# Kernel tuning notes

Hardware: AMD Instinct MI355X
Metric: run time of the kernel (lower is better)

The kernel has to match this reference:

```python
import jax, jax.numpy as jnp
import numpy as np

B, IN, H = 16384, 512, 512


def setup_inputs() -> dict:
    key = jax.random.key(0)
    ks = jax.random.split(key, 7)
    s_in = 1.0 / np.sqrt(IN)
    s_h = 1.0 / np.sqrt(H)
    return {
        "x": jax.random.normal(ks[0], (B, IN), jnp.float32),
        "h": jax.random.normal(ks[1], (B, H), jnp.float32),
        "c": jax.random.normal(ks[2], (B, H), jnp.float32),
        # packed gate weights, order [i, f, g, o] along last dim (4*H)
        "Wx": jax.random.normal(ks[3], (IN, 4 * H), jnp.float32) * s_in,
        "Wh": jax.random.normal(ks[4], (H, 4 * H), jnp.float32) * s_h,
        "bx": jax.random.normal(ks[5], (4 * H,), jnp.float32) * s_in,
        "bh": jax.random.normal(ks[6], (4 * H,), jnp.float32) * s_h,
    }


def reference(x, h, c, Wx, Wh, bx, bh):
    # one fused GEMM per input stream instead of 8 small linears; same math
    gates = x @ Wx + bx + h @ Wh + bh          # [B, 4H]
    gi, gf, gg, go = jnp.split(gates, 4, axis=-1)
    i = jax.nn.sigmoid(gi)
    f = jax.nn.sigmoid(gf)
    g = jnp.tanh(gg)
    o = jax.nn.sigmoid(go)
    c_new = f * c + i * g
    h_new = o * jnp.tanh(c_new)
    return (h_new, c_new)
```

## Files before the change

kernel.cpp:

```cpp
#include <hip/hip_runtime.h>
#include <hip/hip_bf16.h>

#define B_DIM   16384
#define IN_DIM  512
#define H_DIM   512
#define K_DIM   1024
#define N4H     2048
#define BH      (B_DIM * H_DIM)

typedef __attribute__((ext_vector_type(8))) short  short8;
typedef __attribute__((ext_vector_type(4))) short  short4v;
typedef __attribute__((ext_vector_type(4))) float  f32x4;

__device__ inline void async_load16(const void* g, void* l) {
    __builtin_amdgcn_global_load_lds(
        (const __attribute__((address_space(1))) void*)g,
        (__attribute__((address_space(3)))       void*)l, 16, 0, 0);
}

__device__ inline short bf16bits(float f) {
    __hip_bfloat16 b = __float2bfloat16(f);
    return *reinterpret_cast<short*>(&b);
}

__device__ inline float sigmoidf_(float v) {
    return 1.0f / (1.0f + __expf(-v));
}
__device__ inline float tanhf_(float v) {
    v = fminf(fmaxf(v, -30.f), 30.f);
    float e = __expf(2.f * v);
    return (e - 1.f) / (e + 1.f);
}

__global__ __launch_bounds__(256) void prep_all(
    const float* __restrict__ Wx, const float* __restrict__ Wh,
    const float* __restrict__ bx, const float* __restrict__ bh,
    const float* __restrict__ x,  const float* __restrict__ h,
    __hip_bfloat16* __restrict__ Wt, __hip_bfloat16* __restrict__ Axh,
    float* __restrict__ bias_p) {
    const int bid = blockIdx.x;
    const int t   = threadIdx.x;

    if (bid < 2048) {
        __shared__ __hip_bfloat16 tile[32][33];
        const int bk = bid & 31;
        const int bn = bid >> 5;
        const int kb = bk * 32, nb = bn * 32;
#pragma unroll
        for (int r = 0; r < 4; ++r) {
            int k_loc = r * 8 + (t >> 5);
            int n_loc = t & 31;
            int kg = kb + k_loc;
            float v = (kg < IN_DIM) ? Wx[(size_t)kg * N4H + nb + n_loc]
                                    : Wh[(size_t)(kg - IN_DIM) * N4H + nb + n_loc];
            tile[k_loc][n_loc] = __float2bfloat16(v);
        }
        __syncthreads();
        {
            int n_loc = t >> 3;
            int k_loc = (t & 7) * 4;
            int ng = nb + n_loc;
            int g  = ng >> 9;
            int c  = ng & 511;
            int row_out = (c >> 5) * 128 + g * 32 + (c & 31);
            short4v v4;
            v4.x = *reinterpret_cast<short*>(&tile[k_loc + 0][n_loc]);
            v4.y = *reinterpret_cast<short*>(&tile[k_loc + 1][n_loc]);
            v4.z = *reinterpret_cast<short*>(&tile[k_loc + 2][n_loc]);
            v4.w = *reinterpret_cast<short*>(&tile[k_loc + 3][n_loc]);
            *(short4v*)&Wt[(size_t)row_out * K_DIM + kb + k_loc] = v4;
        }
        if (bid < 8) {
            int ng = bid * 256 + t;
            int g  = ng >> 9;
            int c  = ng & 511;
            int ro = (c >> 5) * 128 + g * 32 + (c & 31);
            bias_p[ro] = bx[ng] + bh[ng];
        }
    } else {
        const int ab = bid - 2048;
        const int kq = t;
        const float* src = (kq < 128) ? (x + kq * 4)
                                      : (h + (size_t)(kq - 128) * 4);
#pragma unroll
        for (int j = 0; j < 8; ++j) {
            int m = ab * 8 + j;
            float4 v = *(const float4*)(src + (size_t)m * 512);
            short4v sv;
            sv.x = bf16bits(v.x);
            sv.y = bf16bits(v.y);
            sv.z = bf16bits(v.z);
            sv.w = bf16bits(v.w);
            *(short4v*)&Axh[(size_t)m * K_DIM + kq * 4] = sv;
        }
    }
}

__global__ __launch_bounds__(256, 3) void lstm_gemm(
    const float* __restrict__ c_in,
    const __hip_bfloat16* __restrict__ Axh,
    const __hip_bfloat16* __restrict__ Wt,
    const float* __restrict__ bias_p,
    float* __restrict__ out) {
    __shared__ __hip_bfloat16 lds_a[2][128 * 32];
    __shared__ __hip_bfloat16 lds_b[2][128 * 32];

    const int tid   = threadIdx.x;
    const int w     = tid >> 6;
    const int lane  = tid & 63;
    const int col16 = lane & 15;
    const int quad  = lane >> 4;

    const int jb    = blockIdx.x;
    const int xcd   = jb & 7;
    const int local = jb >> 3;
    const int bm    = xcd * 16 + (local >> 4);
    const int bn    = local & 15;

    f32x4 acc[2][8];
#pragma unroll
    for (int mi = 0; mi < 2; ++mi)
#pragma unroll
        for (int ni = 0; ni < 8; ++ni)
            acc[mi][ni] = (f32x4){0.f, 0.f, 0.f, 0.f};

    const __hip_bfloat16* Ab = Axh + (size_t)bm * 128 * K_DIM;
    const __hip_bfloat16* Bb = Wt  + (size_t)bn * 128 * K_DIM;

    const int s0 = w * 128 + lane;
    const int s1 = s0 + 64;
    const int r0 = s0 >> 2, r1 = s1 >> 2;
    const int q0 = ((s0 & 3) - ((r0 >> 1) & 3)) & 3;
    const int q1 = ((s1 & 3) - ((r1 >> 1) & 3)) & 3;
    const size_t ga0 = (size_t)r0 * K_DIM + q0 * 8;
    const size_t ga1 = (size_t)r1 * K_DIM + q1 * 8;

    int aoff[2], boff[8];
#pragma unroll
    for (int mi = 0; mi < 2; ++mi) {
        int r = w * 32 + mi * 16 + col16;
        aoff[mi] = (r * 4 + ((quad + ((r >> 1) & 3)) & 3)) * 16;
    }
#pragma unroll
    for (int ni = 0; ni < 8; ++ni) {
        int r = ni * 16 + col16;
        boff[ni] = (r * 4 + ((quad + ((r >> 1) & 3)) & 3)) * 16;
    }

    async_load16(Ab + ga0, (void*)(&lds_a[0][w * 1024]));
    async_load16(Ab + ga1, (void*)(&lds_a[0][w * 1024 + 512]));
    async_load16(Bb + ga0, (void*)(&lds_b[0][w * 1024]));
    async_load16(Bb + ga1, (void*)(&lds_b[0][w * 1024 + 512]));

    for (int kt = 0; kt < 32; ++kt) {
        __syncthreads();
        const int p = kt & 1;
        if (kt < 31) {
            const int kb = (kt + 1) * 32;
            async_load16(Ab + ga0 + kb, (void*)(&lds_a[1 - p][w * 1024]));
            async_load16(Ab + ga1 + kb, (void*)(&lds_a[1 - p][w * 1024 + 512]));
            async_load16(Bb + ga0 + kb, (void*)(&lds_b[1 - p][w * 1024]));
            async_load16(Bb + ga1 + kb, (void*)(&lds_b[1 - p][w * 1024 + 512]));
        }
        const char* lap = (const char*)lds_a[p];
        const char* lbp = (const char*)lds_b[p];

        short8 afr[2], bfr[8];
#pragma unroll
        for (int mi = 0; mi < 2; ++mi)
            afr[mi] = *(const short8*)(lap + aoff[mi]);
#pragma unroll
        for (int ni = 0; ni < 8; ++ni)
            bfr[ni] = *(const short8*)(lbp + boff[ni]);
#pragma unroll
        for (int mi = 0; mi < 2; ++mi)
#pragma unroll
            for (int ni = 0; ni < 8; ++ni)
                acc[mi][ni] = __builtin_amdgcn_mfma_f32_16x16x32_bf16(
                    afr[mi], bfr[ni], acc[mi][ni], 0, 0, 0);
    }

    float bias_v[4][2];
#pragma unroll
    for (int g = 0; g < 4; ++g)
#pragma unroll
        for (int h2 = 0; h2 < 2; ++h2)
            bias_v[g][h2] = bias_p[bn * 128 + g * 32 + h2 * 16 + col16];

#pragma unroll
    for (int mi = 0; mi < 2; ++mi) {
#pragma unroll
        for (int reg = 0; reg < 4; ++reg) {
            const int m_g = bm * 128 + w * 32 + mi * 16 + quad * 4 + reg;
#pragma unroll
            for (int h2 = 0; h2 < 2; ++h2) {
                const int hc_g = bn * 32 + h2 * 16 + col16;
                float gi = acc[mi][0 + h2][reg] + bias_v[0][h2];
                float gf = acc[mi][2 + h2][reg] + bias_v[1][h2];
                float gg = acc[mi][4 + h2][reg] + bias_v[2][h2];
                float go = acc[mi][6 + h2][reg] + bias_v[3][h2];
                float iv = sigmoidf_(gi);
                float fv = sigmoidf_(gf);
                float gv = tanhf_(gg);
                float ov = sigmoidf_(go);
                float co = c_in[(size_t)m_g * H_DIM + hc_g];
                float cn = fv * co + iv * gv;
                float hn = ov * tanhf_(cn);
                out[(size_t)m_g * H_DIM + hc_g]      = hn;
                out[BH + (size_t)m_g * H_DIM + hc_g] = cn;
            }
        }
    }
}

__global__ __launch_bounds__(256) void prep_weights_fb(
    const float* __restrict__ Wx, const float* __restrict__ Wh,
    const float* __restrict__ bx, const float* __restrict__ bh,
    __hip_bfloat16* __restrict__ Wt, float* __restrict__ bias_p) {
    __shared__ __hip_bfloat16 tile[32][33];
    const int bid = blockIdx.x;
    const int bk  = bid & 31;
    const int bn  = bid >> 5;
    const int t   = threadIdx.x;
    const int kb  = bk * 32, nb = bn * 32;
#pragma unroll
    for (int r = 0; r < 4; ++r) {
        int k_loc = r * 8 + (t >> 5);
        int n_loc = t & 31;
        int kg = kb + k_loc;
        float v = (kg < IN_DIM) ? Wx[(size_t)kg * N4H + nb + n_loc]
                                : Wh[(size_t)(kg - IN_DIM) * N4H + nb + n_loc];
        tile[k_loc][n_loc] = __float2bfloat16(v);
    }
    __syncthreads();
    {
        int n_loc = t >> 3;
        int k_loc = (t & 7) * 4;
        int ng = nb + n_loc;
        int g  = ng >> 9;
        int c  = ng & 511;
        int row_out = (c >> 5) * 128 + g * 32 + (c & 31);
        short4v v4;
        v4.x = *reinterpret_cast<short*>(&tile[k_loc + 0][n_loc]);
        v4.y = *reinterpret_cast<short*>(&tile[k_loc + 1][n_loc]);
        v4.z = *reinterpret_cast<short*>(&tile[k_loc + 2][n_loc]);
        v4.w = *reinterpret_cast<short*>(&tile[k_loc + 3][n_loc]);
        *(short4v*)&Wt[(size_t)row_out * K_DIM + kb + k_loc] = v4;
    }
    if (bid < 8) {
        int ng = bid * 256 + t;
        int g  = ng >> 9;
        int c  = ng & 511;
        int ro = (c >> 5) * 128 + g * 32 + (c & 31);
        bias_p[ro] = bx[ng] + bh[ng];
    }
}

__global__ __launch_bounds__(256, 3) void lstm_gemm_fb(
    const float* __restrict__ x, const float* __restrict__ h,
    const float* __restrict__ c_in,
    const __hip_bfloat16* __restrict__ Wt, const float* __restrict__ bias_p,
    float* __restrict__ out) {
    __shared__ __hip_bfloat16 lds_a[128 * 32];
    __shared__ __hip_bfloat16 lds_b[128 * 32];
    const int tid   = threadIdx.x;
    const int bn    = blockIdx.x & 15;
    const int bm    = blockIdx.x >> 4;
    const int w     = tid >> 6;
    const int lane  = tid & 63;
    const int col16 = lane & 15;
    const int quad  = lane >> 4;
    f32x4 acc[2][8];
#pragma unroll
    for (int mi = 0; mi < 2; ++mi)
#pragma unroll
        for (int ni = 0; ni < 8; ++ni)
            acc[mi][ni] = (f32x4){0.f, 0.f, 0.f, 0.f};
    const __hip_bfloat16* wt_base = Wt + (size_t)(bn * 128) * K_DIM;
    const int chunk0 = w * 2;
    const int e0     = chunk0 * 512 + lane * 8;
    const int bn_loc0 = e0 >> 5, bk_off0 = e0 & 31;
    const int e1     = (chunk0 + 1) * 512 + lane * 8;
    const int bn_loc1 = e1 >> 5, bk_off1 = e1 & 31;
    for (int kt = 0; kt < 32; ++kt) {
        const int kb = kt * 32;
        const float* aptr;
        int koff;
        if (kb < IN_DIM) { aptr = x; koff = kb; }
        else             { aptr = h; koff = kb - IN_DIM; }
        async_load16(wt_base + (size_t)bn_loc0 * K_DIM + kb + bk_off0,
                     (void*)(lds_b + chunk0 * 512));
        async_load16(wt_base + (size_t)bn_loc1 * K_DIM + kb + bk_off1,
                     (void*)(lds_b + (chunk0 + 1) * 512));
        float4 av[4];
#pragma unroll
        for (int j = 0; j < 4; ++j) {
            int cch = j * 256 + tid;
            int row = cch >> 3;
            int kq  = (cch & 7) * 4;
            av[j] = *(const float4*)(aptr + (size_t)(bm * 128 + row) * IN_DIM
                                     + koff + kq);
        }
#pragma unroll
        for (int j = 0; j < 4; ++j) {
            int cch = j * 256 + tid;
            int row = cch >> 3;
            int kq  = (cch & 7) * 4;
            short4v sv;
            sv.x = bf16bits(av[j].x);
            sv.y = bf16bits(av[j].y);
            sv.z = bf16bits(av[j].z);
            sv.w = bf16bits(av[j].w);
            *(short4v*)&lds_a[row * 32 + kq] = sv;
        }
        __syncthreads();
        short8 afr[2], bfr[8];
#pragma unroll
        for (int mi = 0; mi < 2; ++mi)
            afr[mi] = *(const short8*)&lds_a[(w * 32 + mi * 16 + col16) * 32 + quad * 8];
#pragma unroll
        for (int ni = 0; ni < 8; ++ni)
            bfr[ni] = *(const short8*)&lds_b[(ni * 16 + col16) * 32 + quad * 8];
#pragma unroll
        for (int mi = 0; mi < 2; ++mi)
#pragma unroll
            for (int ni = 0; ni < 8; ++ni)
                acc[mi][ni] = __builtin_amdgcn_mfma_f32_16x16x32_bf16(
                    afr[mi], bfr[ni], acc[mi][ni], 0, 0, 0);
        __syncthreads();
    }
    float bias_v[4][2];
#pragma unroll
    for (int g = 0; g < 4; ++g)
#pragma unroll
        for (int h2 = 0; h2 < 2; ++h2)
            bias_v[g][h2] = bias_p[bn * 128 + g * 32 + h2 * 16 + col16];
#pragma unroll
    for (int mi = 0; mi < 2; ++mi) {
#pragma unroll
        for (int reg = 0; reg < 4; ++reg) {
            const int m_g = bm * 128 + w * 32 + mi * 16 + quad * 4 + reg;
#pragma unroll
            for (int h2 = 0; h2 < 2; ++h2) {
                const int hc_g = bn * 32 + h2 * 16 + col16;
                float gi = acc[mi][0 + h2][reg] + bias_v[0][h2];
                float gf = acc[mi][2 + h2][reg] + bias_v[1][h2];
                float gg = acc[mi][4 + h2][reg] + bias_v[2][h2];
                float go = acc[mi][6 + h2][reg] + bias_v[3][h2];
                float iv = sigmoidf_(gi);
                float fv = sigmoidf_(gf);
                float gv = tanhf_(gg);
                float ov = sigmoidf_(go);
                float co = c_in[(size_t)m_g * H_DIM + hc_g];
                float cn = fv * co + iv * gv;
                float hn = ov * tanhf_(cn);
                out[(size_t)m_g * H_DIM + hc_g]      = hn;
                out[BH + (size_t)m_g * H_DIM + hc_g] = cn;
            }
        }
    }
}

extern "C" void kernel_launch(void* const* d_in, const int* in_sizes, int n_in,
                              void* d_out, int out_size, void* d_ws, size_t ws_size,
                              hipStream_t stream) {
    const float* x  = (const float*)d_in[0];
    const float* h  = (const float*)d_in[1];
    const float* c  = (const float*)d_in[2];
    const float* Wx = (const float*)d_in[3];
    const float* Wh = (const float*)d_in[4];
    const float* bx = (const float*)d_in[5];
    const float* bh = (const float*)d_in[6];

    const size_t wtBytes  = (size_t)N4H * K_DIM * 2;
    const size_t axhBytes = (size_t)B_DIM * K_DIM * 2;
    const size_t need     = wtBytes + axhBytes + (size_t)N4H * 4;

    if (ws_size >= need) {
        __hip_bfloat16* Wt  = (__hip_bfloat16*)d_ws;
        __hip_bfloat16* Axh = (__hip_bfloat16*)((char*)d_ws + wtBytes);
        float* bias_p = (float*)((char*)d_ws + wtBytes + axhBytes);
        prep_all<<<4096, 256, 0, stream>>>(Wx, Wh, bx, bh, x, h, Wt, Axh, bias_p);
        lstm_gemm<<<2048, 256, 0, stream>>>(c, Axh, Wt, bias_p, (float*)d_out);
    } else {
        __hip_bfloat16* Wt = (__hip_bfloat16*)d_ws;
        float* bias_p = (float*)((char*)d_ws + wtBytes);
        prep_weights_fb<<<2048, 256, 0, stream>>>(Wx, Wh, bx, bh, Wt, bias_p);
        lstm_gemm_fb<<<2048, 256, 0, stream>>>(x, h, c, Wt, bias_p, (float*)d_out);
    }
}
```

Before: 246.4 us.

## Fuse fp32-to-bf16 activation conversion into GEMM A-tile loading

The separate pass that converted x and h to a bf16 staging buffer is removed. The GEMM kernel now loads fp32 activations straight into registers, converts them, and writes them to the swizzled LDS double buffer after the MFMA block. This drops a 32MB-write/read round trip and the extra work of 2048 prep blocks. In exchange each GEMM block reads twice as many A bytes, across 16 N-tile blocks, and register pressure rises from holding 4 float4s across the MFMA loop. The fallback path is removed too.

```diff
diff --git a/kernel.cpp b/kernel.cpp
--- a/kernel.cpp
+++ b/kernel.cpp
@@ -32,73 +32,61 @@
     return (e - 1.f) / (e + 1.f);
 }
 
-__global__ __launch_bounds__(256) void prep_all(
+__device__ inline void store_bf16x8(void* dst, float4 a, float4 b) {
+    short8 r;
+    r[0] = bf16bits(a.x); r[1] = bf16bits(a.y);
+    r[2] = bf16bits(a.z); r[3] = bf16bits(a.w);
+    r[4] = bf16bits(b.x); r[5] = bf16bits(b.y);
+    r[6] = bf16bits(b.z); r[7] = bf16bits(b.w);
+    *(short8*)dst = r;
+}
+
+__global__ __launch_bounds__(256) void prep_weights(
     const float* __restrict__ Wx, const float* __restrict__ Wh,
     const float* __restrict__ bx, const float* __restrict__ bh,
+    __hip_bfloat16* __restrict__ Wt, float* __restrict__ bias_p) {
+    __shared__ __hip_bfloat16 tile[32][33];
+    const int bid = blockIdx.x;
+    const int bk  = bid & 31;
+    const int bn  = bid >> 5;
+    const int t   = threadIdx.x;
+    const int kb  = bk * 32, nb = bn * 32;
+#pragma unroll
+    for (int r = 0; r < 4; ++r) {
+        int k_loc = r * 8 + (t >> 5);
+        int n_loc = t & 31;
+        int kg = kb + k_loc;
+        float v = (kg < IN_DIM) ? Wx[(size_t)kg * N4H + nb + n_loc]
+                                : Wh[(size_t)(kg - IN_DIM) * N4H + nb + n_loc];
+        tile[k_loc][n_loc] = __float2bfloat16(v);
+    }
+    __syncthreads();
+    {
+        int n_loc = t >> 3;
+        int k_loc = (t & 7) * 4;
+        int ng = nb + n_loc;
+        int g  = ng >> 9;
+        int c  = ng & 511;
+        int row_out = (c >> 5) * 128 + g * 32 + (c & 31);
+        short4v v4;
+        v4.x = *reinterpret_cast<short*>(&tile[k_loc + 0][n_loc]);
+        v4.y = *reinterpret_cast<short*>(&tile[k_loc + 1][n_loc]);
+        v4.z = *reinterpret_cast<short*>(&tile[k_loc + 2][n_loc]);
+        v4.w = *reinterpret_cast<short*>(&tile[k_loc + 3][n_loc]);
+        *(short4v*)&Wt[(size_t)row_out * K_DIM + kb + k_loc] = v4;
+    }
+    if (bid < 8) {
+        int ng = bid * 256 + t;
+        int g  = ng >> 9;
+        int c  = ng & 511;
+        int ro = (c >> 5) * 128 + g * 32 + (c & 31);
+        bias_p[ro] = bx[ng] + bh[ng];
+    }
+}
+
+__global__ __launch_bounds__(256, 3) void lstm_gemm_fused(
     const float* __restrict__ x,  const float* __restrict__ h,
-    __hip_bfloat16* __restrict__ Wt, __hip_bfloat16* __restrict__ Axh,
-    float* __restrict__ bias_p) {
-    const int bid = blockIdx.x;
-    const int t   = threadIdx.x;
-
-    if (bid < 2048) {
-        __shared__ __hip_bfloat16 tile[32][33];
-        const int bk = bid & 31;
-        const int bn = bid >> 5;
-        const int kb = bk * 32, nb = bn * 32;
-#pragma unroll
-        for (int r = 0; r < 4; ++r) {
-            int k_loc = r * 8 + (t >> 5);
-            int n_loc = t & 31;
-            int kg = kb + k_loc;
-            float v = (kg < IN_DIM) ? Wx[(size_t)kg * N4H + nb + n_loc]
-                                    : Wh[(size_t)(kg - IN_DIM) * N4H + nb + n_loc];
-            tile[k_loc][n_loc] = __float2bfloat16(v);
-        }
-        __syncthreads();
-        {
-            int n_loc = t >> 3;
-            int k_loc = (t & 7) * 4;
-            int ng = nb + n_loc;
-            int g  = ng >> 9;
-            int c  = ng & 511;
-            int row_out = (c >> 5) * 128 + g * 32 + (c & 31);
-            short4v v4;
-            v4.x = *reinterpret_cast<short*>(&tile[k_loc + 0][n_loc]);
-            v4.y = *reinterpret_cast<short*>(&tile[k_loc + 1][n_loc]);
-            v4.z = *reinterpret_cast<short*>(&tile[k_loc + 2][n_loc]);
-            v4.w = *reinterpret_cast<short*>(&tile[k_loc + 3][n_loc]);
-            *(short4v*)&Wt[(size_t)row_out * K_DIM + kb + k_loc] = v4;
-        }
-        if (bid < 8) {
-            int ng = bid * 256 + t;
-            int g  = ng >> 9;
-            int c  = ng & 511;
-            int ro = (c >> 5) * 128 + g * 32 + (c & 31);
-            bias_p[ro] = bx[ng] + bh[ng];
-        }
-    } else {
-        const int ab = bid - 2048;
-        const int kq = t;
-        const float* src = (kq < 128) ? (x + kq * 4)
-                                      : (h + (size_t)(kq - 128) * 4);
-#pragma unroll
-        for (int j = 0; j < 8; ++j) {
-            int m = ab * 8 + j;
-            float4 v = *(const float4*)(src + (size_t)m * 512);
-            short4v sv;
-            sv.x = bf16bits(v.x);
-            sv.y = bf16bits(v.y);
-            sv.z = bf16bits(v.z);
-            sv.w = bf16bits(v.w);
-            *(short4v*)&Axh[(size_t)m * K_DIM + kq * 4] = sv;
-        }
-    }
-}
-
-__global__ __launch_bounds__(256, 3) void lstm_gemm(
     const float* __restrict__ c_in,
-    const __hip_bfloat16* __restrict__ Axh,
     const __hip_bfloat16* __restrict__ Wt,
     const float* __restrict__ bias_p,
     float* __restrict__ out) {
@@ -124,8 +112,9 @@
         for (int ni = 0; ni < 8; ++ni)
             acc[mi][ni] = (f32x4){0.f, 0.f, 0.f, 0.f};
 
-    const __hip_bfloat16* Ab = Axh + (size_t)bm * 128 * K_DIM;
-    const __hip_bfloat16* Bb = Wt  + (size_t)bn * 128 * K_DIM;
+    const __hip_bfloat16* Bb = Wt + (size_t)bn * 128 * K_DIM;
+    const float* xb = x + (size_t)bm * 128 * IN_DIM;
+    const float* hb = h + (size_t)bm * 128 * H_DIM;
 
     const int s0 = w * 128 + lane;
     const int s1 = s0 + 64;
@@ -134,6 +123,8 @@
     const int q1 = ((s1 & 3) - ((r1 >> 1) & 3)) & 3;
     const size_t ga0 = (size_t)r0 * K_DIM + q0 * 8;
     const size_t ga1 = (size_t)r1 * K_DIM + q1 * 8;
+    const size_t ro0 = (size_t)r0 * 512 + q0 * 8;
+    const size_t ro1 = (size_t)r1 * 512 + q1 * 8;
 
     int aoff[2], boff[8];
 #pragma unroll
@@ -147,18 +138,25 @@
         boff[ni] = (r * 4 + ((quad + ((r >> 1) & 3)) & 3)) * 16;
     }
 
-    async_load16(Ab + ga0, (void*)(&lds_a[0][w * 1024]));
-    async_load16(Ab + ga1, (void*)(&lds_a[0][w * 1024 + 512]));
+    float4 A00 = *(const float4*)(xb + ro0);
+    float4 A01 = *(const float4*)(xb + ro0 + 4);
+    float4 A10 = *(const float4*)(xb + ro1);
+    float4 A11 = *(const float4*)(xb + ro1 + 4);
     async_load16(Bb + ga0, (void*)(&lds_b[0][w * 1024]));
     async_load16(Bb + ga1, (void*)(&lds_b[0][w * 1024 + 512]));
+    store_bf16x8((char*)lds_a[0] + s0 * 16, A00, A01);
+    store_bf16x8((char*)lds_a[0] + s1 * 16, A10, A11);
 
     for (int kt = 0; kt < 32; ++kt) {
         __syncthreads();
         const int p = kt & 1;
         if (kt < 31) {
             const int kb = (kt + 1) * 32;
-            async_load16(Ab + ga0 + kb, (void*)(&lds_a[1 - p][w * 1024]));
-            async_load16(Ab + ga1 + kb, (void*)(&lds_a[1 - p][w * 1024 + 512]));
+            const float* sA = (kb < IN_DIM) ? (xb + kb) : (hb + (kb - IN_DIM));
+            A00 = *(const float4*)(sA + ro0);
+            A01 = *(const float4*)(sA + ro0 + 4);
+            A10 = *(const float4*)(sA + ro1);
+            A11 = *(const float4*)(sA + ro1 + 4);
             async_load16(Bb + ga0 + kb, (void*)(&lds_b[1 - p][w * 1024]));
             async_load16(Bb + ga1 + kb, (void*)(&lds_b[1 - p][w * 1024 + 512]));
         }
@@ -178,6 +176,11 @@
             for (int ni = 0; ni < 8; ++ni)
                 acc[mi][ni] = __builtin_amdgcn_mfma_f32_16x16x32_bf16(
                     afr[mi], bfr[ni], acc[mi][ni], 0, 0, 0);
+
+        if (kt < 31) {
+            store_bf16x8((char*)lds_a[1 - p] + s0 * 16, A00, A01);
+            store_bf16x8((char*)lds_a[1 - p] + s1 * 16, A10, A11);
+        }
     }
 
     float bias_v[4][2];
@@ -213,154 +216,6 @@
     }
 }
 
-__global__ __launch_bounds__(256) void prep_weights_fb(
-    const float* __restrict__ Wx, const float* __restrict__ Wh,
-    const float* __restrict__ bx, const float* __restrict__ bh,
-    __hip_bfloat16* __restrict__ Wt, float* __restrict__ bias_p) {
-    __shared__ __hip_bfloat16 tile[32][33];
-    const int bid = blockIdx.x;
-    const int bk  = bid & 31;
-    const int bn  = bid >> 5;
-    const int t   = threadIdx.x;
-    const int kb  = bk * 32, nb = bn * 32;
-#pragma unroll
-    for (int r = 0; r < 4; ++r) {
-        int k_loc = r * 8 + (t >> 5);
-        int n_loc = t & 31;
-        int kg = kb + k_loc;
-        float v = (kg < IN_DIM) ? Wx[(size_t)kg * N4H + nb + n_loc]
-                                : Wh[(size_t)(kg - IN_DIM) * N4H + nb + n_loc];
-        tile[k_loc][n_loc] = __float2bfloat16(v);
-    }
-    __syncthreads();
-    {
-        int n_loc = t >> 3;
-        int k_loc = (t & 7) * 4;
-        int ng = nb + n_loc;
-        int g  = ng >> 9;
-        int c  = ng & 511;
-        int row_out = (c >> 5) * 128 + g * 32 + (c & 31);
-        short4v v4;
-        v4.x = *reinterpret_cast<short*>(&tile[k_loc + 0][n_loc]);
-        v4.y = *reinterpret_cast<short*>(&tile[k_loc + 1][n_loc]);
-        v4.z = *reinterpret_cast<short*>(&tile[k_loc + 2][n_loc]);
-        v4.w = *reinterpret_cast<short*>(&tile[k_loc + 3][n_loc]);
-        *(short4v*)&Wt[(size_t)row_out * K_DIM + kb + k_loc] = v4;
-    }
-    if (bid < 8) {
-        int ng = bid * 256 + t;
-        int g  = ng >> 9;
-        int c  = ng & 511;
-        int ro = (c >> 5) * 128 + g * 32 + (c & 31);
-        bias_p[ro] = bx[ng] + bh[ng];
-    }
-}
-
-__global__ __launch_bounds__(256, 3) void lstm_gemm_fb(
-    const float* __restrict__ x, const float* __restrict__ h,
-    const float* __restrict__ c_in,
-    const __hip_bfloat16* __restrict__ Wt, const float* __restrict__ bias_p,
-    float* __restrict__ out) {
-    __shared__ __hip_bfloat16 lds_a[128 * 32];
-    __shared__ __hip_bfloat16 lds_b[128 * 32];
-    const int tid   = threadIdx.x;
-    const int bn    = blockIdx.x & 15;
-    const int bm    = blockIdx.x >> 4;
-    const int w     = tid >> 6;
-    const int lane  = tid & 63;
-    const int col16 = lane & 15;
-    const int quad  = lane >> 4;
-    f32x4 acc[2][8];
-#pragma unroll
-    for (int mi = 0; mi < 2; ++mi)
-#pragma unroll
-        for (int ni = 0; ni < 8; ++ni)
-            acc[mi][ni] = (f32x4){0.f, 0.f, 0.f, 0.f};
-    const __hip_bfloat16* wt_base = Wt + (size_t)(bn * 128) * K_DIM;
-    const int chunk0 = w * 2;
-    const int e0     = chunk0 * 512 + lane * 8;
-    const int bn_loc0 = e0 >> 5, bk_off0 = e0 & 31;
-    const int e1     = (chunk0 + 1) * 512 + lane * 8;
-    const int bn_loc1 = e1 >> 5, bk_off1 = e1 & 31;
-    for (int kt = 0; kt < 32; ++kt) {
-        const int kb = kt * 32;
-        const float* aptr;
-        int koff;
-        if (kb < IN_DIM) { aptr = x; koff = kb; }
-        else             { aptr = h; koff = kb - IN_DIM; }
-        async_load16(wt_base + (size_t)bn_loc0 * K_DIM + kb + bk_off0,
-                     (void*)(lds_b + chunk0 * 512));
-        async_load16(wt_base + (size_t)bn_loc1 * K_DIM + kb + bk_off1,
-                     (void*)(lds_b + (chunk0 + 1) * 512));
-        float4 av[4];
-#pragma unroll
-        for (int j = 0; j < 4; ++j) {
-            int cch = j * 256 + tid;
-            int row = cch >> 3;
-            int kq  = (cch & 7) * 4;
-            av[j] = *(const float4*)(aptr + (size_t)(bm * 128 + row) * IN_DIM
-                                     + koff + kq);
-        }
-#pragma unroll
-        for (int j = 0; j < 4; ++j) {
-            int cch = j * 256 + tid;
-            int row = cch >> 3;
-            int kq  = (cch & 7) * 4;
-            short4v sv;
-            sv.x = bf16bits(av[j].x);
-            sv.y = bf16bits(av[j].y);
-            sv.z = bf16bits(av[j].z);
-            sv.w = bf16bits(av[j].w);
-            *(short4v*)&lds_a[row * 32 + kq] = sv;
-        }
-        __syncthreads();
-        short8 afr[2], bfr[8];
-#pragma unroll
-        for (int mi = 0; mi < 2; ++mi)
-            afr[mi] = *(const short8*)&lds_a[(w * 32 + mi * 16 + col16) * 32 + quad * 8];
-#pragma unroll
-        for (int ni = 0; ni < 8; ++ni)
-            bfr[ni] = *(const short8*)&lds_b[(ni * 16 + col16) * 32 + quad * 8];
-#pragma unroll
-        for (int mi = 0; mi < 2; ++mi)
-#pragma unroll
-            for (int ni = 0; ni < 8; ++ni)
-                acc[mi][ni] = __builtin_amdgcn_mfma_f32_16x16x32_bf16(
-                    afr[mi], bfr[ni], acc[mi][ni], 0, 0, 0);
-        __syncthreads();
-    }
-    float bias_v[4][2];
-#pragma unroll
-    for (int g = 0; g < 4; ++g)
-#pragma unroll
-        for (int h2 = 0; h2 < 2; ++h2)
-            bias_v[g][h2] = bias_p[bn * 128 + g * 32 + h2 * 16 + col16];
-#pragma unroll
-    for (int mi = 0; mi < 2; ++mi) {
-#pragma unroll
-        for (int reg = 0; reg < 4; ++reg) {
-            const int m_g = bm * 128 + w * 32 + mi * 16 + quad * 4 + reg;
-#pragma unroll
-            for (int h2 = 0; h2 < 2; ++h2) {
-                const int hc_g = bn * 32 + h2 * 16 + col16;
-                float gi = acc[mi][0 + h2][reg] + bias_v[0][h2];
-                float gf = acc[mi][2 + h2][reg] + bias_v[1][h2];
-                float gg = acc[mi][4 + h2][reg] + bias_v[2][h2];
-                float go = acc[mi][6 + h2][reg] + bias_v[3][h2];
-                float iv = sigmoidf_(gi);
-                float fv = sigmoidf_(gf);
-                float gv = tanhf_(gg);
-                float ov = sigmoidf_(go);
-                float co = c_in[(size_t)m_g * H_DIM + hc_g];
-                float cn = fv * co + iv * gv;
-                float hn = ov * tanhf_(cn);
-                out[(size_t)m_g * H_DIM + hc_g]      = hn;
-                out[BH + (size_t)m_g * H_DIM + hc_g] = cn;
-            }
-        }
-    }
-}
-
 extern "C" void kernel_launch(void* const* d_in, const int* in_sizes, int n_in,
                               void* d_out, int out_size, void* d_ws, size_t ws_size,
                               hipStream_t stream) {
@@ -372,20 +227,10 @@
     const float* bx = (const float*)d_in[5];
     const float* bh = (const float*)d_in[6];
 
-    const size_t wtBytes  = (size_t)N4H * K_DIM * 2;
-    const size_t axhBytes = (size_t)B_DIM * K_DIM * 2;
-    const size_t need     = wtBytes + axhBytes + (size_t)N4H * 4;
-
-    if (ws_size >= need) {
-        __hip_bfloat16* Wt  = (__hip_bfloat16*)d_ws;
-        __hip_bfloat16* Axh = (__hip_bfloat16*)((char*)d_ws + wtBytes);
-        float* bias_p = (float*)((char*)d_ws + wtBytes + axhBytes);
-        prep_all<<<4096, 256, 0, stream>>>(Wx, Wh, bx, bh, x, h, Wt, Axh, bias_p);
-        lstm_gemm<<<2048, 256, 0, stream>>>(c, Axh, Wt, bias_p, (float*)d_out);
-    } else {
-        __hip_bfloat16* Wt = (__hip_bfloat16*)d_ws;
-        float* bias_p = (float*)((char*)d_ws + wtBytes);
-        prep_weights_fb<<<2048, 256, 0, stream>>>(Wx, Wh, bx, bh, Wt, bias_p);
-        lstm_gemm_fb<<<2048, 256, 0, stream>>>(x, h, c, Wt, bias_p, (float*)d_out);
-    }
-}
+    const size_t wtBytes = (size_t)N4H * K_DIM * 2;
+    __hip_bfloat16* Wt = (__hip_bfloat16*)d_ws;
+    float* bias_p = (float*)((char*)d_ws + wtBytes);
+
+    prep_weights<<<2048, 256, 0, stream>>>(Wx, Wh, bx, bh, Wt, bias_p);
+    lstm_gemm_fused<<<2048, 256, 0, stream>>>(x, h, c, Wt, bias_p, (float*)d_out);
+}
```

Result: slower. 282.3 us (+14.6%).

## Use 256x128 tiles with 8 waves and triple-buffered BK=64 pipeline

Applied to the files above, without the earlier changes.

Replaces the 128x128, 4-wave GEMM with a 256x128 tile computed by 8 waves in a 4x2 grid. K tiles grow to 64 and the LDS pipeline goes from two buffers to three, with explicit vmcnt waits so two stages of loads stay in flight. The LDS layout switches to an XOR swizzle, and MFMA blocks are wrapped in setprio. This is meant to raise arithmetic intensity and hide global latency, at the cost of more LDS (144KB), fewer blocks per CU, and a smaller grid.

```diff
diff --git a/kernel.cpp b/kernel.cpp
--- a/kernel.cpp
+++ b/kernel.cpp
@@ -96,119 +96,132 @@
     }
 }
 
-__global__ __launch_bounds__(256, 3) void lstm_gemm(
+__global__ __launch_bounds__(512, 2) void lstm_gemm8t(
     const float* __restrict__ c_in,
     const __hip_bfloat16* __restrict__ Axh,
     const __hip_bfloat16* __restrict__ Wt,
     const float* __restrict__ bias_p,
     float* __restrict__ out) {
-    __shared__ __hip_bfloat16 lds_a[2][128 * 32];
-    __shared__ __hip_bfloat16 lds_b[2][128 * 32];
+    __shared__ __align__(16) __hip_bfloat16 lds_a[3][16384];
+    __shared__ __align__(16) __hip_bfloat16 lds_b[3][8192];
 
     const int tid   = threadIdx.x;
     const int w     = tid >> 6;
     const int lane  = tid & 63;
     const int col16 = lane & 15;
     const int quad  = lane >> 4;
+    const int wm    = w >> 1;
+    const int wnn   = w & 1;
 
     const int jb    = blockIdx.x;
     const int xcd   = jb & 7;
     const int local = jb >> 3;
-    const int bm    = xcd * 16 + (local >> 4);
+    const int bm    = xcd * 8 + (local >> 4);
     const int bn    = local & 15;
 
-    f32x4 acc[2][8];
-#pragma unroll
-    for (int mi = 0; mi < 2; ++mi)
-#pragma unroll
-        for (int ni = 0; ni < 8; ++ni)
+    f32x4 acc[4][4];
+#pragma unroll
+    for (int mi = 0; mi < 4; ++mi)
+#pragma unroll
+        for (int ni = 0; ni < 4; ++ni)
             acc[mi][ni] = (f32x4){0.f, 0.f, 0.f, 0.f};
 
-    const __hip_bfloat16* Ab = Axh + (size_t)bm * 128 * K_DIM;
+    const __hip_bfloat16* Ab = Axh + (size_t)bm * 256 * K_DIM;
     const __hip_bfloat16* Bb = Wt  + (size_t)bn * 128 * K_DIM;
 
-    const int s0 = w * 128 + lane;
-    const int s1 = s0 + 64;
-    const int r0 = s0 >> 2, r1 = s1 >> 2;
-    const int q0 = ((s0 & 3) - ((r0 >> 1) & 3)) & 3;
-    const int q1 = ((s1 & 3) - ((r1 >> 1) & 3)) & 3;
-    const size_t ga0 = (size_t)r0 * K_DIM + q0 * 8;
-    const size_t ga1 = (size_t)r1 * K_DIM + q1 * 8;
-
-    int aoff[2], boff[8];
-#pragma unroll
-    for (int mi = 0; mi < 2; ++mi) {
-        int r = w * 32 + mi * 16 + col16;
-        aoff[mi] = (r * 4 + ((quad + ((r >> 1) & 3)) & 3)) * 16;
-    }
-#pragma unroll
-    for (int ni = 0; ni < 8; ++ni) {
-        int r = ni * 16 + col16;
-        boff[ni] = (r * 4 + ((quad + ((r >> 1) & 3)) & 3)) * 16;
-    }
-
-    async_load16(Ab + ga0, (void*)(&lds_a[0][w * 1024]));
-    async_load16(Ab + ga1, (void*)(&lds_a[0][w * 1024 + 512]));
-    async_load16(Bb + ga0, (void*)(&lds_b[0][w * 1024]));
-    async_load16(Bb + ga1, (void*)(&lds_b[0][w * 1024 + 512]));
-
-    for (int kt = 0; kt < 32; ++kt) {
-        __syncthreads();
-        const int p = kt & 1;
-        if (kt < 31) {
-            const int kb = (kt + 1) * 32;
-            async_load16(Ab + ga0 + kb, (void*)(&lds_a[1 - p][w * 1024]));
-            async_load16(Ab + ga1 + kb, (void*)(&lds_a[1 - p][w * 1024 + 512]));
-            async_load16(Bb + ga0 + kb, (void*)(&lds_b[1 - p][w * 1024]));
-            async_load16(Bb + ga1 + kb, (void*)(&lds_b[1 - p][w * 1024 + 512]));
-        }
-        const char* lap = (const char*)lds_a[p];
-        const char* lbp = (const char*)lds_b[p];
-
-        short8 afr[2], bfr[8];
-#pragma unroll
-        for (int mi = 0; mi < 2; ++mi)
-            afr[mi] = *(const short8*)(lap + aoff[mi]);
-#pragma unroll
-        for (int ni = 0; ni < 8; ++ni)
-            bfr[ni] = *(const short8*)(lbp + boff[ni]);
-#pragma unroll
-        for (int mi = 0; mi < 2; ++mi)
-#pragma unroll
-            for (int ni = 0; ni < 8; ++ni)
-                acc[mi][ni] = __builtin_amdgcn_mfma_f32_16x16x32_bf16(
-                    afr[mi], bfr[ni], acc[mi][ni], 0, 0, 0);
-    }
-
-    float bias_v[4][2];
+    const int rsub = lane >> 3;
+    const int lg   = (lane & 7) ^ rsub;
+
+    auto STAGE = [&](int buf, int kt) {
+        char* ba = (char*)lds_a[buf] + w * 1024;
+        char* bb = (char*)lds_b[buf] + w * 1024;
+        const __hip_bfloat16* As = Ab + (size_t)(w * 8 + rsub) * K_DIM + kt * 64 + lg * 8;
+        const __hip_bfloat16* Bs = Bb + (size_t)(w * 8 + rsub) * K_DIM + kt * 64 + lg * 8;
+        async_load16(As,                      ba);
+        async_load16(As +  64 * K_DIM,        ba + 8192);
+        async_load16(As + 128 * K_DIM,        ba + 16384);
+        async_load16(As + 192 * K_DIM,        ba + 24576);
+        async_load16(Bs,                      bb);
+        async_load16(Bs +  64 * K_DIM,        bb + 8192);
+    };
+
+    int arow[4], brow[4], kx[2];
+#pragma unroll
+    for (int mi = 0; mi < 4; ++mi)
+        arow[mi] = (wm * 64 + mi * 16 + col16) * 128;
+#pragma unroll
+    for (int ni = 0; ni < 4; ++ni)
+        brow[ni] = (ni * 32 + wnn * 16 + col16) * 128;
+#pragma unroll
+    for (int ks = 0; ks < 2; ++ks)
+        kx[ks] = (ks * 64 + quad * 16) ^ ((col16 & 7) << 4);
+
+    STAGE(0, 0);
+    STAGE(1, 1);
+
+    int cur = 0;
+    for (int t = 0; t < 16; ++t) {
+        if (t < 15) asm volatile("s_waitcnt vmcnt(6)" ::: "memory");
+        else        asm volatile("s_waitcnt vmcnt(0)" ::: "memory");
+        __builtin_amdgcn_s_barrier();
+        __builtin_amdgcn_sched_barrier(0);
+
+        if (t < 14) {
+            const int nxt = (cur >= 1) ? cur - 1 : 2;
+            STAGE(nxt, t + 2);
+        }
+
+        const char* la = (const char*)lds_a[cur];
+        const char* lb = (const char*)lds_b[cur];
+
+#pragma unroll
+        for (int ks = 0; ks < 2; ++ks) {
+            short8 afr[4], bfr[4];
+#pragma unroll
+            for (int mi = 0; mi < 4; ++mi)
+                afr[mi] = *(const short8*)(la + arow[mi] + kx[ks]);
+#pragma unroll
+            for (int ni = 0; ni < 4; ++ni)
+                bfr[ni] = *(const short8*)(lb + brow[ni] + kx[ks]);
+
+            __builtin_amdgcn_s_setprio(1);
+#pragma unroll
+            for (int mi = 0; mi < 4; ++mi)
+#pragma unroll
+                for (int ni = 0; ni < 4; ++ni)
+                    acc[mi][ni] = __builtin_amdgcn_mfma_f32_16x16x32_bf16(
+                        afr[mi], bfr[ni], acc[mi][ni], 0, 0, 0);
+            __builtin_amdgcn_s_setprio(0);
+        }
+
+        cur = (cur == 2) ? 0 : cur + 1;
+    }
+
+    float bias_v[4];
 #pragma unroll
     for (int g = 0; g < 4; ++g)
-#pragma unroll
-        for (int h2 = 0; h2 < 2; ++h2)
-            bias_v[g][h2] = bias_p[bn * 128 + g * 32 + h2 * 16 + col16];
-
-#pragma unroll
-    for (int mi = 0; mi < 2; ++mi) {
+        bias_v[g] = bias_p[bn * 128 + g * 32 + wnn * 16 + col16];
+
+    const int hc_g = bn * 32 + wnn * 16 + col16;
+
+#pragma unroll
+    for (int mi = 0; mi < 4; ++mi) {
 #pragma unroll
         for (int reg = 0; reg < 4; ++reg) {
-            const int m_g = bm * 128 + w * 32 + mi * 16 + quad * 4 + reg;
-#pragma unroll
-            for (int h2 = 0; h2 < 2; ++h2) {
-                const int hc_g = bn * 32 + h2 * 16 + col16;
-                float gi = acc[mi][0 + h2][reg] + bias_v[0][h2];
-                float gf = acc[mi][2 + h2][reg] + bias_v[1][h2];
-                float gg = acc[mi][4 + h2][reg] + bias_v[2][h2];
-                float go = acc[mi][6 + h2][reg] + bias_v[3][h2];
-                float iv = sigmoidf_(gi);
-                float fv = sigmoidf_(gf);
-                float gv = tanhf_(gg);
-                float ov = sigmoidf_(go);
-                float co = c_in[(size_t)m_g * H_DIM + hc_g];
-                float cn = fv * co + iv * gv;
-                float hn = ov * tanhf_(cn);
-                out[(size_t)m_g * H_DIM + hc_g]      = hn;
-                out[BH + (size_t)m_g * H_DIM + hc_g] = cn;
-            }
+            const int m_g = bm * 256 + wm * 64 + mi * 16 + quad * 4 + reg;
+            float gi = acc[mi][0][reg] + bias_v[0];
+            float gf = acc[mi][1][reg] + bias_v[1];
+            float gg = acc[mi][2][reg] + bias_v[2];
+            float go = acc[mi][3][reg] + bias_v[3];
+            float iv = sigmoidf_(gi);
+            float fv = sigmoidf_(gf);
+            float gv = tanhf_(gg);
+            float ov = sigmoidf_(go);
+            float co = c_in[(size_t)m_g * H_DIM + hc_g];
+            float cn = fv * co + iv * gv;
+            float hn = ov * tanhf_(cn);
+            out[(size_t)m_g * H_DIM + hc_g]      = hn;
+            out[BH + (size_t)m_g * H_DIM + hc_g] = cn;
         }
     }
 }
@@ -381,7 +394,7 @@
         __hip_bfloat16* Axh = (__hip_bfloat16*)((char*)d_ws + wtBytes);
         float* bias_p = (float*)((char*)d_ws + wtBytes + axhBytes);
         prep_all<<<4096, 256, 0, stream>>>(Wx, Wh, bx, bh, x, h, Wt, Axh, bias_p);
-        lstm_gemm<<<2048, 256, 0, stream>>>(c, Axh, Wt, bias_p, (float*)d_out);
+        lstm_gemm8t<<<1024, 512, 0, stream>>>(c, Axh, Wt, bias_p, (float*)d_out);
     } else {
         __hip_bfloat16* Wt = (__hip_bfloat16*)d_ws;
         float* bias_p = (float*)((char*)d_ws + wtBytes);
```

After: 261.3 us. 1.06x slower.
